# Kernel optimization log

Hardware: AMD Instinct MI355X
Metric: run time of the kernel (lower is better)

## Reference

```python
import jax, jax.numpy as jnp
import numpy as np

# M5-style dims
N = 30490          # nodes (3049 items x 10 stores)
E = 487840         # edges (~16 avg degree)
T = 90             # time steps (largest signature window)
C = 2              # input channels
WINDOWS = (7, 28, 90)
H, DH, HID, L, ET = 4, 32, 128, 3, 3   # heads, head_dim, gat hidden, layers, edge types
HOR, NG = 28, 7
MAX_RATIO = 20.0
D_LL = 2 * C                                  # lead-lag channel count
SIG_PER_WIN = D_LL + D_LL**2 + D_LL**3        # depth-3 signature dim = 84
SIG_DIM = len(WINDOWS) * SIG_PER_WIN          # 252
EMB_DIM = 8 + 8 + 4 + 4 + 16                  # 40


def _lead_lag(x):
    # (N, T, C) -> (N, 2T-1, 2C) standard lead-lag path augmentation
    xr = jnp.repeat(x, 2, axis=1)
    return jnp.concatenate([xr[:, 1:, :], xr[:, :-1, :]], axis=-1)


def _sig3(path):
    # exact truncated (depth-3) path signature of a piecewise-linear path (N, M+1, d)
    dx = path[:, 1:] - path[:, :-1]                      # (N, M, d)
    n, _, d = dx.shape
    c1 = jnp.cumsum(dx, axis=1) - dx                     # exclusive cumsum: S1 before step i
    s1 = dx.sum(axis=1)                                  # (N, d)
    inc2 = c1[..., :, None] * dx[..., None, :] + 0.5 * dx[..., :, None] * dx[..., None, :]
    c2 = jnp.cumsum(inc2, axis=1) - inc2                 # exclusive S2 before step i (N,M,d,d)
    s2 = inc2.sum(axis=1)                                # (N, d, d)
    # Chen: S3 += S2<i (x) dx + S1<i (x) dx(x)dx / 2 + dx(x)dx(x)dx / 6
    s3 = (jnp.einsum('nmab,nmc->nabc', c2, dx)
          + 0.5 * jnp.einsum('nma,nmb,nmc->nabc', c1, dx, dx)
          + jnp.einsum('nma,nmb,nmc->nabc', dx, dx, dx) / 6.0)
    return jnp.concatenate([s1, s2.reshape(n, d * d), s3.reshape(n, d * d * d)], axis=-1)


def _signature_features(x):
    return jnp.concatenate([_sig3(_lead_lag(x[:, -w:, :])) for w in WINDOWS], axis=-1)


def _layer_norm(x, g, b):
    m = x.mean(axis=-1, keepdims=True)
    v = ((x - m) ** 2).mean(axis=-1, keepdims=True)
    return (x - m) / jnp.sqrt(v + 1e-5) * g + b


def _gat_layer(h, src, dst, etype, W, b, a_src, a_dst, et_bias, Wres):
    n = h.shape[0]
    q = (h @ W + b).reshape(n, H, DH)                    # (N, H, DH)
    es = (q * a_src).sum(-1)                             # (N, H)
    ed = (q * a_dst).sum(-1)
    logit = jax.nn.leaky_relu(es[src] + ed[dst] + et_bias[etype], 0.2)   # (E, H)
    m = jax.lax.stop_gradient(jax.ops.segment_max(logit, dst, num_segments=n))
    m = jnp.where(jnp.isfinite(m), m, 0.0)
    ex = jnp.exp(logit - m[dst])
    den = jax.ops.segment_sum(ex, dst, num_segments=n)
    alpha = ex / (den[dst] + 1e-9)                       # per-destination softmax
    msg = jax.ops.segment_sum(alpha[:, :, None] * q[src], dst, num_segments=n)
    return jax.nn.elu(msg.reshape(n, H * DH) + h @ Wres)  # residual


def _forward(fl, edge_index, edge_type, store_id, dept_id, cat_id, state_id, item_id, dept_ids):
    (node_features, historical_mean, emb_store, emb_dept, emb_cat, emb_state, emb_item,
     fusion_W, fusion_b, ln_g, ln_b, gat_W, gat_b, gat_asrc, gat_adst, gat_et, gat_Wres,
     pred_W1, pred_b1, pred_W2, pred_b2, pred_W3, pred_b3, horizon_scale, group_scale) = fl
    sig = _signature_features(node_features)             # (N, 252)
    cat = jnp.concatenate([emb_store[store_id], emb_dept[dept_id], emb_cat[cat_id],
                           emb_state[state_id], emb_item[item_id]], axis=-1)  # (N, 40)
    h = jnp.concatenate([sig, cat], axis=-1)
    h = _layer_norm(jax.nn.gelu(h @ fusion_W + fusion_b, approximate=False), ln_g, ln_b)
    src, dst = edge_index[0], edge_index[1]
    for i in range(L):
        h = _gat_layer(h, src, dst, edge_type, gat_W[i], gat_b[i],
                       gat_asrc[i], gat_adst[i], gat_et[i], gat_Wres[i])
    x = jax.nn.gelu(h @ pred_W1 + pred_b1, approximate=False)
    x = jax.nn.gelu(x @ pred_W2 + pred_b2, approximate=False)
    pred = (x @ pred_W3 + pred_b3) * jax.nn.softplus(horizon_scale)
    # simple reconciliation: per-group learnable scale + clip by historical mean
    pred = pred * jax.nn.softplus(group_scale)[dept_ids][:, None]
    pred = jnp.clip(pred, 0.0, MAX_RATIO * historical_mean[:, None])
    return pred


def setup_inputs() -> dict:
    keys = iter(jax.random.split(jax.random.key(0), 40))
    def nrm(shape, s=0.05):
        return jax.random.normal(next(keys), shape, jnp.float32) * s
    inp = {}
    inp['node_features'] = jax.random.normal(next(keys), (N, T, C), jnp.float32)
    inp['edge_index'] = jax.random.randint(next(keys), (2, E), 0, N)
    inp['edge_type'] = jax.random.randint(next(keys), (E,), 0, ET)
    inp['store_id'] = jax.random.randint(next(keys), (N,), 0, 10)
    inp['dept_id'] = jax.random.randint(next(keys), (N,), 0, 7)
    inp['cat_id'] = jax.random.randint(next(keys), (N,), 0, 3)
    inp['state_id'] = jax.random.randint(next(keys), (N,), 0, 3)
    inp['item_id'] = jax.random.randint(next(keys), (N,), 0, 3049)
    inp['dept_ids'] = jax.random.randint(next(keys), (N,), 0, NG)
    inp['historical_mean'] = jax.random.uniform(next(keys), (N,), jnp.float32)
    # parameters
    inp['emb_store'] = nrm((10, 8), 0.1)
    inp['emb_dept'] = nrm((7, 8), 0.1)
    inp['emb_cat'] = nrm((3, 4), 0.1)
    inp['emb_state'] = nrm((3, 4), 0.1)
    inp['emb_item'] = nrm((3049, 16), 0.1)
    inp['fusion_W'] = nrm((SIG_DIM + EMB_DIM, HID))
    inp['fusion_b'] = jnp.zeros((HID,), jnp.float32)
    inp['ln_g'] = jnp.ones((HID,), jnp.float32)
    inp['ln_b'] = jnp.zeros((HID,), jnp.float32)
    inp['gat_W'] = nrm((L, HID, HID))
    inp['gat_b'] = jnp.zeros((L, HID), jnp.float32)
    inp['gat_asrc'] = nrm((L, H, DH), 0.1)
    inp['gat_adst'] = nrm((L, H, DH), 0.1)
    inp['gat_et'] = nrm((L, ET, H), 0.1)
    inp['gat_Wres'] = nrm((L, HID, HID))
    inp['pred_W1'] = nrm((HID, 256))
    inp['pred_b1'] = jnp.zeros((256,), jnp.float32)
    inp['pred_W2'] = nrm((256, 256))
    inp['pred_b2'] = jnp.zeros((256,), jnp.float32)
    inp['pred_W3'] = nrm((256, HOR))
    inp['pred_b3'] = jnp.zeros((HOR,), jnp.float32)
    inp['horizon_scale'] = jnp.ones((HOR,), jnp.float32)
    inp['group_scale'] = jnp.ones((NG,), jnp.float32)
    return inp


def reference(node_features, edge_index, edge_type, store_id, dept_id, cat_id, state_id,
              item_id, dept_ids, historical_mean, emb_store, emb_dept, emb_cat, emb_state,
              emb_item, fusion_W, fusion_b, ln_g, ln_b, gat_W, gat_b, gat_asrc, gat_adst,
              gat_et, gat_Wres, pred_W1, pred_b1, pred_W2, pred_b2, pred_W3, pred_b3,
              horizon_scale, group_scale):
    fl = (node_features, historical_mean, emb_store, emb_dept, emb_cat, emb_state, emb_item,
          fusion_W, fusion_b, ln_g, ln_b, gat_W, gat_b, gat_asrc, gat_adst, gat_et, gat_Wres,
          pred_W1, pred_b1, pred_W2, pred_b2, pred_W3, pred_b3, horizon_scale, group_scale)
    return _forward(fl, edge_index, edge_type, store_id, dept_id, cat_id, state_id, item_id, dept_ids)
```

## Files before the change

### kernel.cpp

```cpp
#include <hip/hip_runtime.h>
#include <math.h>

#define HID 128
#define DHD 32
#define N_T 90

__device__ __forceinline__ float gelu_f(float x) {
    return 0.5f * x * (1.0f + erff(x * 0.70710678118654752f));
}
__device__ __forceinline__ float softplus_f(float x) {
    return fmaxf(x, 0.0f) + log1pf(expf(-fabsf(x)));
}

template<int P>
__device__ __forceinline__ void sig_substep(float c1[4], float c2[16], float s3[64],
                                            float d0, float d1) {
    float h00 = 0.5f * d0 * d0, h01 = 0.5f * d0 * d1, h11 = 0.5f * d1 * d1;
#pragma unroll
    for (int a = 0; a < 4; ++a) {
#pragma unroll
        for (int b = 0; b < 4; ++b) {
            float c2ab = c2[a * 4 + b];
            s3[a * 16 + b * 4 + P + 0] += c2ab * d0;
            s3[a * 16 + b * 4 + P + 1] += c2ab * d1;
        }
    }
#pragma unroll
    for (int a = 0; a < 4; ++a) {
        float c = c1[a];
        s3[a * 16 + (P + 0) * 4 + (P + 0)] += c * h00;
        s3[a * 16 + (P + 0) * 4 + (P + 1)] += c * h01;
        s3[a * 16 + (P + 1) * 4 + (P + 0)] += c * h01;
        s3[a * 16 + (P + 1) * 4 + (P + 1)] += c * h11;
    }
    const float i6 = 0.16666666666666666f;
    float t000 = d0 * d0 * d0 * i6, t001 = d0 * d0 * d1 * i6;
    float t011 = d0 * d1 * d1 * i6, t111 = d1 * d1 * d1 * i6;
    s3[(P + 0) * 16 + (P + 0) * 4 + (P + 0)] += t000;
    s3[(P + 0) * 16 + (P + 0) * 4 + (P + 1)] += t001;
    s3[(P + 0) * 16 + (P + 1) * 4 + (P + 0)] += t001;
    s3[(P + 0) * 16 + (P + 1) * 4 + (P + 1)] += t011;
    s3[(P + 1) * 16 + (P + 0) * 4 + (P + 0)] += t001;
    s3[(P + 1) * 16 + (P + 0) * 4 + (P + 1)] += t011;
    s3[(P + 1) * 16 + (P + 1) * 4 + (P + 0)] += t011;
    s3[(P + 1) * 16 + (P + 1) * 4 + (P + 1)] += t111;
#pragma unroll
    for (int a = 0; a < 4; ++a) {
        float c = c1[a];
        c2[a * 4 + P + 0] += c * d0;
        c2[a * 4 + P + 1] += c * d1;
    }
    c2[(P + 0) * 4 + (P + 0)] += h00;
    c2[(P + 0) * 4 + (P + 1)] += h01;
    c2[(P + 1) * 4 + (P + 0)] += h01;
    c2[(P + 1) * 4 + (P + 1)] += h11;
    c1[P + 0] += d0;
    c1[P + 1] += d1;
}

__global__ void sig_kernel(const float* __restrict__ nf, float* __restrict__ X, int nn) {
    int node = blockIdx.x * blockDim.x + threadIdx.x;
    int win = blockIdx.y;
    if (node >= nn) return;
    int w = (win == 0) ? 7 : (win == 1) ? 28 : 90;
    const float* xp = nf + (size_t)node * (N_T * 2) + (size_t)(N_T - w) * 2;
    float c1[4] = {0.f, 0.f, 0.f, 0.f};
    float c2[16] = {0.f};
    float s3[64] = {0.f};
    float p0 = xp[0], p1 = xp[1];
    for (int i = 1; i < w; ++i) {
        float n0 = xp[i * 2], n1 = xp[i * 2 + 1];
        float d0 = n0 - p0, d1 = n1 - p1;
        sig_substep<0>(c1, c2, s3, d0, d1);
        sig_substep<2>(c1, c2, s3, d0, d1);
        p0 = n0; p1 = n1;
    }
    float* o = X + (size_t)node * 292 + win * 84;
#pragma unroll
    for (int k = 0; k < 4; ++k) o[k] = c1[k];
#pragma unroll
    for (int k = 0; k < 16; ++k) o[4 + k] = c2[k];
#pragma unroll
    for (int k = 0; k < 64; ++k) o[20 + k] = s3[k];
}

__global__ void emb_kernel(float* __restrict__ X,
                           const int* __restrict__ store_id, const int* __restrict__ dept_id,
                           const int* __restrict__ cat_id, const int* __restrict__ state_id,
                           const int* __restrict__ item_id,
                           const float* __restrict__ e_store, const float* __restrict__ e_dept,
                           const float* __restrict__ e_cat, const float* __restrict__ e_state,
                           const float* __restrict__ e_item, int nn) {
    int n = blockIdx.x * blockDim.x + threadIdx.x;
    if (n >= nn) return;
    float* o = X + (size_t)n * 292 + 252;
    const float* p;
    p = e_store + store_id[n] * 8;
#pragma unroll
    for (int j = 0; j < 8; ++j) o[j] = p[j];
    p = e_dept + dept_id[n] * 8;
#pragma unroll
    for (int j = 0; j < 8; ++j) o[8 + j] = p[j];
    p = e_cat + cat_id[n] * 4;
#pragma unroll
    for (int j = 0; j < 4; ++j) o[16 + j] = p[j];
    p = e_state + state_id[n] * 4;
#pragma unroll
    for (int j = 0; j < 4; ++j) o[20 + j] = p[j];
    p = e_item + item_id[n] * 16;
#pragma unroll
    for (int j = 0; j < 16; ++j) o[24 + j] = p[j];
}

__global__ __launch_bounds__(256)
void gemm_kernel(const float* __restrict__ A, const float* __restrict__ B,
                 const float* __restrict__ bias, float* __restrict__ C,
                 int M, int N, int K, int act) {
    __shared__ float As[16][68];
    __shared__ float Bs[16][68];
    int tid = threadIdx.x;
    int bm = blockIdx.x * 64;
    int bn = blockIdx.y * 64;
    int tx = tid & 15, ty = tid >> 4;
    int ar = tid >> 2, ac = (tid & 3) * 4;
    int br = tid >> 4, bc = (tid & 15) * 4;
    float acc[4][4] = {};
    for (int k0 = 0; k0 < K; k0 += 16) {
        float av[4] = {0.f, 0.f, 0.f, 0.f};
        int grow = bm + ar;
        if (grow < M) {
            int gc = k0 + ac;
            if (gc + 4 <= K) {
                const float4 v = *(const float4*)(A + (size_t)grow * K + gc);
                av[0] = v.x; av[1] = v.y; av[2] = v.z; av[3] = v.w;
            } else {
                for (int u = 0; u < 4; ++u)
                    if (gc + u < K) av[u] = A[(size_t)grow * K + gc + u];
            }
        }
        float bv[4] = {0.f, 0.f, 0.f, 0.f};
        int brow = k0 + br;
        if (brow < K) {
            int gc = bn + bc;
            if (gc + 4 <= N) {
                const float4 v = *(const float4*)(B + (size_t)brow * N + gc);
                bv[0] = v.x; bv[1] = v.y; bv[2] = v.z; bv[3] = v.w;
            } else {
                for (int u = 0; u < 4; ++u)
                    if (gc + u < N) bv[u] = B[(size_t)brow * N + gc + u];
            }
        }
        __syncthreads();
        As[ac + 0][ar] = av[0];
        As[ac + 1][ar] = av[1];
        As[ac + 2][ar] = av[2];
        As[ac + 3][ar] = av[3];
        *(float4*)&Bs[br][bc] = make_float4(bv[0], bv[1], bv[2], bv[3]);
        __syncthreads();
#pragma unroll
        for (int kk = 0; kk < 16; ++kk) {
            float4 a = *(const float4*)&As[kk][ty * 4];
            float4 b = *(const float4*)&Bs[kk][tx * 4];
            float aa[4] = {a.x, a.y, a.z, a.w};
            float bb[4] = {b.x, b.y, b.z, b.w};
#pragma unroll
            for (int i = 0; i < 4; ++i)
#pragma unroll
                for (int j = 0; j < 4; ++j) acc[i][j] += aa[i] * bb[j];
        }
    }
#pragma unroll
    for (int i = 0; i < 4; ++i) {
        int row = bm + ty * 4 + i;
        if (row >= M) continue;
        int col0 = bn + tx * 4;
        float v[4];
#pragma unroll
        for (int j = 0; j < 4; ++j) {
            float x = acc[i][j];
            int col = col0 + j;
            if (col < N && bias) x += bias[col];
            if (act == 1) x = gelu_f(x);
            v[j] = x;
        }
        if (col0 + 4 <= N) {
            *(float4*)(C + (size_t)row * N + col0) = make_float4(v[0], v[1], v[2], v[3]);
        } else {
            for (int j = 0; j < 4; ++j)
                if (col0 + j < N) C[(size_t)row * N + col0 + j] = v[j];
        }
    }
}

__global__ void gelu_ln_kernel(float* __restrict__ h, const float* __restrict__ g,
                               const float* __restrict__ b) {
    int row = blockIdx.x, t = threadIdx.x;
    float* hp = h + (size_t)row * HID;
    float x = gelu_f(hp[t]);
    __shared__ float red[2];
    float s = x;
#pragma unroll
    for (int off = 32; off > 0; off >>= 1) s += __shfl_xor(s, off);
    if ((t & 63) == 0) red[t >> 6] = s;
    __syncthreads();
    float mean = (red[0] + red[1]) * (1.0f / 128.0f);
    float d = x - mean;
    float vs = d * d;
    __syncthreads();
#pragma unroll
    for (int off = 32; off > 0; off >>= 1) vs += __shfl_xor(vs, off);
    if ((t & 63) == 0) red[t >> 6] = vs;
    __syncthreads();
    float var = (red[0] + red[1]) * (1.0f / 128.0f);
    hp[t] = d / sqrtf(var + 1e-5f) * g[t] + b[t];
}

__global__ void hist_kernel(const int* __restrict__ dst, int* __restrict__ deg, int e) {
    int i = blockIdx.x * blockDim.x + threadIdx.x;
    if (i < e) atomicAdd(&deg[dst[i]], 1);
}

__global__ void scan_kernel(const int* __restrict__ deg, int* __restrict__ row_start,
                            int* __restrict__ cursor, int n) {
    __shared__ int wsum[16];
    __shared__ int chunk_total;
    int t = threadIdx.x;
    int lane = t & 63, wv = t >> 6;
    int carry = 0;
    for (int base = 0; base < n; base += 1024) {
        int i = base + t;
        int d = (i < n) ? deg[i] : 0;
        int v = d;
#pragma unroll
        for (int off = 1; off < 64; off <<= 1) {
            int u = __shfl_up(v, off);
            if (lane >= off) v += u;
        }
        if (lane == 63) wsum[wv] = v;
        __syncthreads();
        if (t == 0) {
            int acc2 = 0;
#pragma unroll
            for (int k = 0; k < 16; ++k) {
                int tmp = wsum[k];
                wsum[k] = acc2;
                acc2 += tmp;
            }
            chunk_total = acc2;
        }
        __syncthreads();
        int excl = v - d + wsum[wv] + carry;
        if (i < n) {
            row_start[i] = excl;
            cursor[i] = excl;
        }
        carry += chunk_total;
        __syncthreads();
    }
    if (t == 0) row_start[n] = carry;
}

__global__ void scatter_kernel(const int* __restrict__ src, const int* __restrict__ dst,
                               const int* __restrict__ et, int* __restrict__ cursor,
                               int* __restrict__ csr, int e) {
    int i = blockIdx.x * blockDim.x + threadIdx.x;
    if (i < e) {
        int d = dst[i];
        int pos = atomicAdd(&cursor[d], 1);
        csr[pos] = src[i] | (et[i] << 20);
    }
}

__global__ void esed_kernel(const float* __restrict__ q, const float* __restrict__ asrc,
                            const float* __restrict__ adst, float* __restrict__ es,
                            float* __restrict__ ed, int nn) {
    int idx = blockIdx.x * blockDim.x + threadIdx.x;
    if (idx >= nn * 4) return;
    int n = idx >> 2, hh = idx & 3;
    const float* qp = q + (size_t)n * HID + hh * DHD;
    const float* ap = asrc + hh * DHD;
    const float* dp = adst + hh * DHD;
    float s = 0.f, d = 0.f;
#pragma unroll
    for (int k = 0; k < DHD; ++k) {
        float qv = qp[k];
        s += qv * ap[k];
        d += qv * dp[k];
    }
    es[idx] = s;
    ed[idx] = d;
}

__global__ void gat_agg_kernel(const float* __restrict__ q, const float* __restrict__ r,
                               const float* __restrict__ es, const float* __restrict__ ed,
                               const float* __restrict__ etb,
                               const int* __restrict__ row_start, const int* __restrict__ csr,
                               float* __restrict__ hout, int nn) {
    int n = blockIdx.x;
    int t = threadIdx.x;
    int hh = t >> 5;
    float b0 = etb[0 * 4 + hh], b1 = etb[1 * 4 + hh], b2 = etb[2 * 4 + hh];
    float edn = ed[n * 4 + hh];
    int e0 = row_start[n], e1 = row_start[n + 1];
    float m = -INFINITY, den = 0.f, acc = 0.f;
    for (int e = e0; e < e1; ++e) {
        int info = csr[e];
        int s = info & 0xFFFFF;
        int et = info >> 20;
        float lg = es[s * 4 + hh] + edn + (et == 0 ? b0 : (et == 1 ? b1 : b2));
        lg = lg > 0.f ? lg : 0.2f * lg;
        float qv = q[(size_t)s * HID + t];
        float nm = fmaxf(m, lg);
        float corr = expf(m - nm);
        float p = expf(lg - nm);
        den = den * corr + p;
        acc = acc * corr + p * qv;
        m = nm;
    }
    float msg = acc / (den + 1e-9f);
    float v = msg + r[(size_t)n * HID + t];
    hout[(size_t)n * HID + t] = v > 0.f ? v : expm1f(v);
}

__global__ void final_kernel(const float* __restrict__ y, const float* __restrict__ hs,
                             const float* __restrict__ gs, const int* __restrict__ dept_ids,
                             const float* __restrict__ hm, float* __restrict__ out, int nn) {
    int idx = blockIdx.x * blockDim.x + threadIdx.x;
    if (idx >= nn * 28) return;
    int n = idx / 28, j = idx - n * 28;
    float v = y[idx] * softplus_f(hs[j]) * softplus_f(gs[dept_ids[n]]);
    float hi = 20.0f * hm[n];
    out[idx] = fminf(fmaxf(v, 0.0f), hi);
}

extern "C" void kernel_launch(void* const* d_in, const int* in_sizes, int n_in,
                              void* d_out, int out_size, void* d_ws, size_t ws_size,
                              hipStream_t stream) {
    const float* nf       = (const float*)d_in[0];
    const int*   eidx     = (const int*)d_in[1];
    const int*   etype    = (const int*)d_in[2];
    const int*   store_id = (const int*)d_in[3];
    const int*   dept_id  = (const int*)d_in[4];
    const int*   cat_id   = (const int*)d_in[5];
    const int*   state_id = (const int*)d_in[6];
    const int*   item_id  = (const int*)d_in[7];
    const int*   dept_ids = (const int*)d_in[8];
    const float* hm       = (const float*)d_in[9];
    const float* e_store  = (const float*)d_in[10];
    const float* e_dept   = (const float*)d_in[11];
    const float* e_cat    = (const float*)d_in[12];
    const float* e_state  = (const float*)d_in[13];
    const float* e_item   = (const float*)d_in[14];
    const float* fusion_W = (const float*)d_in[15];
    const float* fusion_b = (const float*)d_in[16];
    const float* ln_g     = (const float*)d_in[17];
    const float* ln_b     = (const float*)d_in[18];
    const float* gat_W    = (const float*)d_in[19];
    const float* gat_b    = (const float*)d_in[20];
    const float* gat_asrc = (const float*)d_in[21];
    const float* gat_adst = (const float*)d_in[22];
    const float* gat_et   = (const float*)d_in[23];
    const float* gat_Wres = (const float*)d_in[24];
    const float* pW1      = (const float*)d_in[25];
    const float* pb1      = (const float*)d_in[26];
    const float* pW2      = (const float*)d_in[27];
    const float* pb2      = (const float*)d_in[28];
    const float* pW3      = (const float*)d_in[29];
    const float* pb3      = (const float*)d_in[30];
    const float* hs       = (const float*)d_in[31];
    const float* gs       = (const float*)d_in[32];

    const int nn = in_sizes[3];
    const int ee = in_sizes[2];
    const int* src = eidx;
    const int* dst = eidx + ee;

    float* ws = (float*)d_ws;
    float* X  = ws;
    float* h  = X + (size_t)nn * 292;
    float* q  = h + (size_t)nn * 128;
    float* r  = q + (size_t)nn * 128;
    float* t2 = r + (size_t)nn * 128;
    float* es = t2 + (size_t)nn * 256;
    float* ed = es + (size_t)nn * 4;
    int* deg       = (int*)(ed + (size_t)nn * 4);
    int* row_start = deg + nn;
    int* cursor    = row_start + nn + 1;
    int* csr       = cursor + nn;
    float* t1 = X;
    float* y  = q;

    hipMemsetAsync(deg, 0, nn * sizeof(int), stream);
    hist_kernel<<<(ee + 255) / 256, 256, 0, stream>>>(dst, deg, ee);
    scan_kernel<<<1, 1024, 0, stream>>>(deg, row_start, cursor, nn);
    scatter_kernel<<<(ee + 255) / 256, 256, 0, stream>>>(src, dst, etype, cursor, csr, ee);

    dim3 sg((nn + 255) / 256, 3);
    sig_kernel<<<sg, 256, 0, stream>>>(nf, X, nn);
    emb_kernel<<<(nn + 255) / 256, 256, 0, stream>>>(X, store_id, dept_id, cat_id, state_id,
                                                     item_id, e_store, e_dept, e_cat, e_state,
                                                     e_item, nn);

    dim3 g1((nn + 63) / 64, 2);
    gemm_kernel<<<g1, 256, 0, stream>>>(X, fusion_W, fusion_b, h, nn, 128, 292, 0);
    gelu_ln_kernel<<<nn, 128, 0, stream>>>(h, ln_g, ln_b);

    for (int l = 0; l < 3; ++l) {
        gemm_kernel<<<g1, 256, 0, stream>>>(h, gat_W + (size_t)l * 128 * 128,
                                            gat_b + l * 128, q, nn, 128, 128, 0);
        gemm_kernel<<<g1, 256, 0, stream>>>(h, gat_Wres + (size_t)l * 128 * 128,
                                            nullptr, r, nn, 128, 128, 0);
        esed_kernel<<<(nn * 4 + 255) / 256, 256, 0, stream>>>(q, gat_asrc + l * 128,
                                                              gat_adst + l * 128, es, ed, nn);
        gat_agg_kernel<<<nn, 128, 0, stream>>>(q, r, es, ed, gat_et + l * 12,
                                               row_start, csr, h, nn);
    }

    dim3 g2((nn + 63) / 64, 4);
    gemm_kernel<<<g2, 256, 0, stream>>>(h, pW1, pb1, t1, nn, 256, 128, 1);
    gemm_kernel<<<g2, 256, 0, stream>>>(t1, pW2, pb2, t2, nn, 256, 256, 1);
    dim3 g3((nn + 63) / 64, 1);
    gemm_kernel<<<g3, 256, 0, stream>>>(t2, pW3, pb3, y, nn, 28, 256, 0);
    final_kernel<<<(nn * 28 + 255) / 256, 256, 0, stream>>>(y, hs, gs, dept_ids, hm,
                                                            (float*)d_out, nn);
}
```

Baseline: 837.4 us.

## Use 128-row GEMM tiles, precompute edge softmax, and widen the CSR scan

Adds a 128x64-tile GEMM kernel with 8x4 per-thread accumulators and uses it for the fusion, GAT and first two predictor GEMMs, to raise arithmetic intensity. The per-node online softmax in GAT aggregation is split into separate per-edge logit, per-node max/denominator and per-edge alpha kernels, so the aggregation loop becomes a plain weighted sum. The scan kernel now handles 8 elements per thread to cut serial iterations. In exchange there are three extra kernel launches per layer and an extra per-edge float4 buffer that is written and read again.

New measurement: 926.2 us. 1.11x slower.

```diff
diff --git a/kernel.cpp b/kernel.cpp
--- a/kernel.cpp
+++ b/kernel.cpp
@@ -110,6 +110,97 @@
     p = e_item + item_id[n] * 16;
 #pragma unroll
     for (int j = 0; j < 16; ++j) o[24 + j] = p[j];
+}
+
+__global__ __launch_bounds__(256)
+void gemm128_kernel(const float* __restrict__ A, const float* __restrict__ B,
+                    const float* __restrict__ bias, float* __restrict__ C,
+                    int M, int N, int K, int act) {
+    __shared__ float As[16][132];
+    __shared__ float Bs[16][68];
+    int tid = threadIdx.x;
+    int bm = blockIdx.x * 128;
+    int bn = blockIdx.y * 64;
+    int tx = tid & 15, ty = tid >> 4;
+    int ar = tid >> 2, ac = (tid & 3) * 4;
+    int br = tid >> 4, bc = (tid & 15) * 4;
+    float acc[8][4] = {};
+    for (int k0 = 0; k0 < K; k0 += 16) {
+        float av0[4] = {0.f, 0.f, 0.f, 0.f};
+        float av1[4] = {0.f, 0.f, 0.f, 0.f};
+        float bv[4]  = {0.f, 0.f, 0.f, 0.f};
+        int gc = k0 + ac;
+        int r0 = bm + ar, r1 = bm + ar + 64;
+        if (gc + 4 <= K) {
+            if (r0 < M) {
+                float4 v = *(const float4*)(A + (size_t)r0 * K + gc);
+                av0[0] = v.x; av0[1] = v.y; av0[2] = v.z; av0[3] = v.w;
+            }
+            if (r1 < M) {
+                float4 v = *(const float4*)(A + (size_t)r1 * K + gc);
+                av1[0] = v.x; av1[1] = v.y; av1[2] = v.z; av1[3] = v.w;
+            }
+        } else {
+            for (int u = 0; u < 4; ++u) {
+                if (gc + u < K) {
+                    if (r0 < M) av0[u] = A[(size_t)r0 * K + gc + u];
+                    if (r1 < M) av1[u] = A[(size_t)r1 * K + gc + u];
+                }
+            }
+        }
+        int brow = k0 + br;
+        if (brow < K) {
+            int gcB = bn + bc;
+            if (gcB + 4 <= N) {
+                float4 v = *(const float4*)(B + (size_t)brow * N + gcB);
+                bv[0] = v.x; bv[1] = v.y; bv[2] = v.z; bv[3] = v.w;
+            } else {
+                for (int u = 0; u < 4; ++u)
+                    if (gcB + u < N) bv[u] = B[(size_t)brow * N + gcB + u];
+            }
+        }
+        __syncthreads();
+#pragma unroll
+        for (int u = 0; u < 4; ++u) {
+            As[ac + u][ar] = av0[u];
+            As[ac + u][ar + 64] = av1[u];
+        }
+        *(float4*)&Bs[br][bc] = make_float4(bv[0], bv[1], bv[2], bv[3]);
+        __syncthreads();
+#pragma unroll
+        for (int kk = 0; kk < 16; ++kk) {
+            float4 a0 = *(const float4*)&As[kk][ty * 8];
+            float4 a1 = *(const float4*)&As[kk][ty * 8 + 4];
+            float4 b  = *(const float4*)&Bs[kk][tx * 4];
+            float aa[8] = {a0.x, a0.y, a0.z, a0.w, a1.x, a1.y, a1.z, a1.w};
+            float bb[4] = {b.x, b.y, b.z, b.w};
+#pragma unroll
+            for (int i = 0; i < 8; ++i)
+#pragma unroll
+                for (int j = 0; j < 4; ++j) acc[i][j] += aa[i] * bb[j];
+        }
+    }
+#pragma unroll
+    for (int i = 0; i < 8; ++i) {
+        int row = bm + ty * 8 + i;
+        if (row >= M) continue;
+        int col0 = bn + tx * 4;
+        float v[4];
+#pragma unroll
+        for (int j = 0; j < 4; ++j) {
+            float x = acc[i][j];
+            int col = col0 + j;
+            if (col < N && bias) x += bias[col];
+            if (act == 1) x = gelu_f(x);
+            v[j] = x;
+        }
+        if (col0 + 4 <= N) {
+            *(float4*)(C + (size_t)row * N + col0) = make_float4(v[0], v[1], v[2], v[3]);
+        } else {
+            for (int j = 0; j < 4; ++j)
+                if (col0 + j < N) C[(size_t)row * N + col0 + j] = v[j];
+        }
+    }
 }
 
 __global__ __launch_bounds__(256)
@@ -227,32 +318,42 @@
     int t = threadIdx.x;
     int lane = t & 63, wv = t >> 6;
     int carry = 0;
-    for (int base = 0; base < n; base += 1024) {
-        int i = base + t;
-        int d = (i < n) ? deg[i] : 0;
-        int v = d;
+    for (int base = 0; base < n; base += 8192) {
+        int idx0 = base + t * 8;
+        int v[8];
+        int s = 0;
+#pragma unroll
+        for (int u = 0; u < 8; ++u) {
+            int d = (idx0 + u < n) ? deg[idx0 + u] : 0;
+            v[u] = s;
+            s += d;
+        }
+        int ws = s;
 #pragma unroll
         for (int off = 1; off < 64; off <<= 1) {
-            int u = __shfl_up(v, off);
-            if (lane >= off) v += u;
-        }
-        if (lane == 63) wsum[wv] = v;
+            int u2 = __shfl_up(ws, off);
+            if (lane >= off) ws += u2;
+        }
+        if (lane == 63) wsum[wv] = ws;
         __syncthreads();
         if (t == 0) {
-            int acc2 = 0;
+            int a = 0;
 #pragma unroll
             for (int k = 0; k < 16; ++k) {
                 int tmp = wsum[k];
-                wsum[k] = acc2;
-                acc2 += tmp;
-            }
-            chunk_total = acc2;
-        }
-        __syncthreads();
-        int excl = v - d + wsum[wv] + carry;
-        if (i < n) {
-            row_start[i] = excl;
-            cursor[i] = excl;
+                wsum[k] = a;
+                a += tmp;
+            }
+            chunk_total = a;
+        }
+        __syncthreads();
+        int excl = ws - s + wsum[wv] + carry;
+#pragma unroll
+        for (int u = 0; u < 8; ++u) {
+            if (idx0 + u < n) {
+                row_start[idx0 + u] = excl + v[u];
+                cursor[idx0 + u] = excl + v[u];
+            }
         }
         carry += chunk_total;
         __syncthreads();
@@ -262,12 +363,13 @@
 
 __global__ void scatter_kernel(const int* __restrict__ src, const int* __restrict__ dst,
                                const int* __restrict__ et, int* __restrict__ cursor,
-                               int* __restrict__ csr, int e) {
+                               int* __restrict__ csr_src, int* __restrict__ csr_de, int e) {
     int i = blockIdx.x * blockDim.x + threadIdx.x;
     if (i < e) {
         int d = dst[i];
         int pos = atomicAdd(&cursor[d], 1);
-        csr[pos] = src[i] | (et[i] << 20);
+        csr_src[pos] = src[i];
+        csr_de[pos] = d | (et[i] << 20);
     }
 }
 
@@ -291,34 +393,71 @@
     ed[idx] = d;
 }
 
+__global__ void lg_kernel(const int* __restrict__ csr_src, const int* __restrict__ csr_de,
+                          const float* __restrict__ es, const float* __restrict__ ed,
+                          const float* __restrict__ etb, float* __restrict__ lg_csr, int e) {
+    int pos = blockIdx.x * blockDim.x + threadIdx.x;
+    if (pos >= e) return;
+    int s = csr_src[pos];
+    int de = csr_de[pos];
+    int d = de & 0xFFFFF;
+    int et = de >> 20;
+    float4 esv = *(const float4*)(es + (size_t)s * 4);
+    float4 edv = *(const float4*)(ed + (size_t)d * 4);
+    float4 bv  = *(const float4*)(etb + (size_t)et * 4);
+    float l0 = esv.x + edv.x + bv.x;
+    float l1 = esv.y + edv.y + bv.y;
+    float l2 = esv.z + edv.z + bv.z;
+    float l3 = esv.w + edv.w + bv.w;
+    l0 = l0 > 0.f ? l0 : 0.2f * l0;
+    l1 = l1 > 0.f ? l1 : 0.2f * l1;
+    l2 = l2 > 0.f ? l2 : 0.2f * l2;
+    l3 = l3 > 0.f ? l3 : 0.2f * l3;
+    *(float4*)(lg_csr + (size_t)pos * 4) = make_float4(l0, l1, l2, l3);
+}
+
+__global__ void mden_kernel(const float* __restrict__ lg_csr, const int* __restrict__ row_start,
+                            float* __restrict__ m_arr, float* __restrict__ den_arr, int nn) {
+    int idx = blockIdx.x * blockDim.x + threadIdx.x;
+    if (idx >= nn * 4) return;
+    int n = idx >> 2, hh = idx & 3;
+    int e0 = row_start[n], e1 = row_start[n + 1];
+    float m = -INFINITY;
+    for (int e = e0; e < e1; ++e) m = fmaxf(m, lg_csr[(size_t)e * 4 + hh]);
+    if (e0 == e1) m = 0.f;
+    float den = 0.f;
+    for (int e = e0; e < e1; ++e) den += expf(lg_csr[(size_t)e * 4 + hh] - m);
+    m_arr[idx] = m;
+    den_arr[idx] = den;
+}
+
+__global__ void alpha_kernel(float* __restrict__ lg_csr, const int* __restrict__ csr_de,
+                             const float* __restrict__ m_arr, const float* __restrict__ den_arr,
+                             int e) {
+    int idx = blockIdx.x * blockDim.x + threadIdx.x;
+    if (idx >= e * 4) return;
+    int pos = idx >> 2, hh = idx & 3;
+    int d = csr_de[pos] & 0xFFFFF;
+    float a = expf(lg_csr[idx] - m_arr[(size_t)d * 4 + hh]) /
+              (den_arr[(size_t)d * 4 + hh] + 1e-9f);
+    lg_csr[idx] = a;
+}
+
 __global__ void gat_agg_kernel(const float* __restrict__ q, const float* __restrict__ r,
-                               const float* __restrict__ es, const float* __restrict__ ed,
-                               const float* __restrict__ etb,
-                               const int* __restrict__ row_start, const int* __restrict__ csr,
+                               const float* __restrict__ alpha_csr,
+                               const int* __restrict__ row_start, const int* __restrict__ csr_src,
                                float* __restrict__ hout, int nn) {
     int n = blockIdx.x;
     int t = threadIdx.x;
     int hh = t >> 5;
-    float b0 = etb[0 * 4 + hh], b1 = etb[1 * 4 + hh], b2 = etb[2 * 4 + hh];
-    float edn = ed[n * 4 + hh];
     int e0 = row_start[n], e1 = row_start[n + 1];
-    float m = -INFINITY, den = 0.f, acc = 0.f;
+    float acc = 0.f;
     for (int e = e0; e < e1; ++e) {
-        int info = csr[e];
-        int s = info & 0xFFFFF;
-        int et = info >> 20;
-        float lg = es[s * 4 + hh] + edn + (et == 0 ? b0 : (et == 1 ? b1 : b2));
-        lg = lg > 0.f ? lg : 0.2f * lg;
-        float qv = q[(size_t)s * HID + t];
-        float nm = fmaxf(m, lg);
-        float corr = expf(m - nm);
-        float p = expf(lg - nm);
-        den = den * corr + p;
-        acc = acc * corr + p * qv;
-        m = nm;
-    }
-    float msg = acc / (den + 1e-9f);
-    float v = msg + r[(size_t)n * HID + t];
+        int s = csr_src[e];
+        float al = alpha_csr[(size_t)e * 4 + hh];
+        acc += al * q[(size_t)s * HID + t];
+    }
+    float v = acc + r[(size_t)n * HID + t];
     hout[(size_t)n * HID + t] = v > 0.f ? v : expm1f(v);
 }
 
@@ -376,24 +515,29 @@
     const int* dst = eidx + ee;
 
     float* ws = (float*)d_ws;
-    float* X  = ws;
-    float* h  = X + (size_t)nn * 292;
-    float* q  = h + (size_t)nn * 128;
-    float* r  = q + (size_t)nn * 128;
-    float* t2 = r + (size_t)nn * 128;
-    float* es = t2 + (size_t)nn * 256;
-    float* ed = es + (size_t)nn * 4;
-    int* deg       = (int*)(ed + (size_t)nn * 4);
+    float* X   = ws;
+    float* h   = X + (size_t)nn * 292;
+    float* q   = h + (size_t)nn * 128;
+    float* r   = q + (size_t)nn * 128;
+    float* t2  = r + (size_t)nn * 128;
+    float* es  = t2 + (size_t)nn * 256;
+    float* ed  = es + (size_t)nn * 4;
+    float* m_a = ed + (size_t)nn * 4;
+    float* d_a = m_a + (size_t)nn * 4;
+    float* lg  = d_a + (size_t)nn * 4;
+    int* deg       = (int*)(lg + (size_t)ee * 4);
     int* row_start = deg + nn;
     int* cursor    = row_start + nn + 1;
-    int* csr       = cursor + nn;
+    int* csr_src   = cursor + nn;
+    int* csr_de    = csr_src + ee;
     float* t1 = X;
     float* y  = q;
 
     hipMemsetAsync(deg, 0, nn * sizeof(int), stream);
     hist_kernel<<<(ee + 255) / 256, 256, 0, stream>>>(dst, deg, ee);
     scan_kernel<<<1, 1024, 0, stream>>>(deg, row_start, cursor, nn);
-    scatter_kernel<<<(ee + 255) / 256, 256, 0, stream>>>(src, dst, etype, cursor, csr, ee);
+    scatter_kernel<<<(ee + 255) / 256, 256, 0, stream>>>(src, dst, etype, cursor,
+                                                         csr_src, csr_de, ee);
 
     dim3 sg((nn + 255) / 256, 3);
     sig_kernel<<<sg, 256, 0, stream>>>(nf, X, nn);
@@ -401,24 +545,27 @@
                                                      item_id, e_store, e_dept, e_cat, e_state,
                                                      e_item, nn);
 
-    dim3 g1((nn + 63) / 64, 2);
-    gemm_kernel<<<g1, 256, 0, stream>>>(X, fusion_W, fusion_b, h, nn, 128, 292, 0);
+    dim3 g128_2((nn + 127) / 128, 2);
+    gemm128_kernel<<<g128_2, 256, 0, stream>>>(X, fusion_W, fusion_b, h, nn, 128, 292, 0);
     gelu_ln_kernel<<<nn, 128, 0, stream>>>(h, ln_g, ln_b);
 
     for (int l = 0; l < 3; ++l) {
-        gemm_kernel<<<g1, 256, 0, stream>>>(h, gat_W + (size_t)l * 128 * 128,
-                                            gat_b + l * 128, q, nn, 128, 128, 0);
-        gemm_kernel<<<g1, 256, 0, stream>>>(h, gat_Wres + (size_t)l * 128 * 128,
-                                            nullptr, r, nn, 128, 128, 0);
+        gemm128_kernel<<<g128_2, 256, 0, stream>>>(h, gat_W + (size_t)l * 128 * 128,
+                                                   gat_b + l * 128, q, nn, 128, 128, 0);
+        gemm128_kernel<<<g128_2, 256, 0, stream>>>(h, gat_Wres + (size_t)l * 128 * 128,
+                                                   nullptr, r, nn, 128, 128, 0);
         esed_kernel<<<(nn * 4 + 255) / 256, 256, 0, stream>>>(q, gat_asrc + l * 128,
                                                               gat_adst + l * 128, es, ed, nn);
-        gat_agg_kernel<<<nn, 128, 0, stream>>>(q, r, es, ed, gat_et + l * 12,
-                                               row_start, csr, h, nn);
-    }
-
-    dim3 g2((nn + 63) / 64, 4);
-    gemm_kernel<<<g2, 256, 0, stream>>>(h, pW1, pb1, t1, nn, 256, 128, 1);
-    gemm_kernel<<<g2, 256, 0, stream>>>(t1, pW2, pb2, t2, nn, 256, 256, 1);
+        lg_kernel<<<(ee + 255) / 256, 256, 0, stream>>>(csr_src, csr_de, es, ed,
+                                                        gat_et + l * 12, lg, ee);
+        mden_kernel<<<(nn * 4 + 255) / 256, 256, 0, stream>>>(lg, row_start, m_a, d_a, nn);
+        alpha_kernel<<<(ee * 4 + 255) / 256, 256, 0, stream>>>(lg, csr_de, m_a, d_a, ee);
+        gat_agg_kernel<<<nn, 128, 0, stream>>>(q, r, lg, row_start, csr_src, h, nn);
+    }
+
+    dim3 g128_4((nn + 127) / 128, 4);
+    gemm128_kernel<<<g128_4, 256, 0, stream>>>(h, pW1, pb1, t1, nn, 256, 128, 1);
+    gemm128_kernel<<<g128_4, 256, 0, stream>>>(t1, pW2, pb2, t2, nn, 256, 256, 1);
     dim3 g3((nn + 63) / 64, 1);
     gemm_kernel<<<g3, 256, 0, stream>>>(t2, pW3, pb3, y, nn, 28, 256, 0);
     final_kernel<<<(nn * 28 + 255) / 256, 256, 0, stream>>>(y, hs, gs, dept_ids, hm,
```
